# Optimization experiments

Measured on AMD Instinct MI355X. Metric: run time of the kernel, lower is better.

The kernel has to match this reference:

```python
import jax, jax.numpy as jnp
import numpy as np

N = 4_194_304      # number of coordinate samples
H = 4              # hidden_features
L = 256            # hidden_layers
FIRST_OMEGA = 3000.0
HIDDEN_OMEGA = 30.0


def setup_inputs() -> dict:
    key = jax.random.key(0)
    ks = jax.random.split(key, 11)
    coords = jax.random.normal(ks[0], (N, 1), dtype=jnp.float32)
    # first layer: weight uniform(-1/in_features, 1/in_features), in_features=1
    w_first = jax.random.uniform(ks[1], (H, 1), jnp.float32, -1.0, 1.0)
    b_first = jax.random.uniform(ks[2], (H,), jnp.float32, -1.0, 1.0)
    # hidden layers: uniform(-sqrt(6/H)/omega, +)
    c_hid = float(np.sqrt(6.0 / H) / HIDDEN_OMEGA)
    w_hidden = jax.random.uniform(ks[3], (L, H, H), jnp.float32, -c_hid, c_hid)
    b_hidden = jax.random.uniform(ks[4], (L, H), jnp.float32, -c_hid, c_hid)
    # outermost linear, same init const
    w_out = jax.random.uniform(ks[5], (1, H), jnp.float32, -c_hid, c_hid)
    b_out = jax.random.uniform(ks[6], (1,), jnp.float32, -c_hid, c_hid)
    # harmonizer scalars (a,b,c,d); near 0 so exp(a)~1
    a_param = (jax.random.normal(ks[7], (), jnp.float32) * 0.1)
    b_param = (jax.random.normal(ks[8], (), jnp.float32) * 0.1)
    c_param = (jax.random.normal(ks[9], (), jnp.float32) * 0.1)
    d_param = (jax.random.normal(ks[10], (), jnp.float32) * 0.1)
    return {
        "coords": coords,
        "w_first": w_first, "b_first": b_first,
        "w_hidden": w_hidden, "b_hidden": b_hidden,
        "w_out": w_out, "b_out": b_out,
        "a_param": a_param, "b_param": b_param,
        "c_param": c_param, "d_param": d_param,
    }


def reference(coords, w_first, b_first, w_hidden, b_hidden, w_out, b_out,
              a_param, b_param, c_param, d_param):
    amp = jnp.exp(a_param)
    freq = jnp.exp(b_param)
    # first sine layer, omega_0 = 3000
    x = amp * jnp.sin(freq * FIRST_OMEGA * (coords @ w_first.T + b_first) + c_param) + d_param
    # 256 hidden sine layers, omega_0 = 30, via scan over the stacked weights
    def step(h, wb):
        W, bvec = wb  # W: [H,H], bvec: [H]
        h = amp * jnp.sin(freq * HIDDEN_OMEGA * (h @ W.T + bvec) + c_param) + d_param
        return h, None
    x, _ = jax.lax.scan(step, x, (w_hidden, b_hidden))
    # outermost plain linear
    return x @ w_out.T + b_out
```

## Files before the change

### kernel.cpp

```cpp
#include <hip/hip_runtime.h>
#include <math.h>

#define NSAMP 4194304
#define LAYERS 256
#define SPT 8


__global__ void prep_kernel(
    const float* __restrict__ w_hidden, const float* __restrict__ b_hidden,
    const float* __restrict__ w_out,   const float* __restrict__ b_out,
    const float* __restrict__ a_param, const float* __restrict__ b_param,
    const float* __restrict__ c_param, const float* __restrict__ d_param,
    float* __restrict__ ws)
{
  const double TWO_PI = 6.283185307179586476925286766559;
  int idx = blockIdx.x * blockDim.x + threadIdx.x;
  float freqf = (float)exp((double)b_param[0]);
  float gf = (float)((double)freqf * 30.0);
  double scale = (double)gf / TWO_PI;
  if (idx < 4096) {
    ws[16 + idx] = (float)((double)w_hidden[idx] * scale);
  } else if (idx < 5120) {
    int bi = idx - 4096;
    ws[16 + 4096 + bi] =
        (float)(((double)gf * (double)b_hidden[bi] + (double)c_param[0]) / TWO_PI);
  } else if (idx == 5120) {
    ws[0] = (float)exp((double)a_param[0]);
    ws[1] = d_param[0];
    ws[2] = (float)((double)freqf * 3000.0);
    ws[3] = c_param[0];
    ws[4] = b_out[0];
    ws[5] = w_out[0]; ws[6] = w_out[1]; ws[7] = w_out[2]; ws[8] = w_out[3];
  }
}

#if defined(__has_builtin)
#if __has_builtin(__builtin_amdgcn_sinf)
#define HAVE_SINF_BUILTIN 1
#endif
#endif

__device__ __forceinline__ float vsin_rev(float x) {
#ifdef HAVE_SINF_BUILTIN
  return __builtin_amdgcn_sinf(x);
#else
  float r;
  asm("v_sin_f32 %0, %1" : "=v"(r) : "v"(x));
  return r;
#endif
}

__device__ __forceinline__ float sin_first(float A) {
  double x = (double)A;
  double kd = rint(x * 0.31830988618379067154);
  double r  = fma(-kd, 3.1415926535897931159979634685, x);
  r = fma(-kd, 1.2246467991473531772e-16, r);
  double r2 = r * r;
  double p = 1.6059043836821613e-10;
  p = fma(r2, p, -2.5052108385441718775e-8);
  p = fma(r2, p,  2.7557319223985890653e-6);
  p = fma(r2, p, -1.9841269841269841270e-4);
  p = fma(r2, p,  8.3333333333333333333e-3);
  p = fma(r2, p, -1.6666666666666666667e-1);
  double s = fma(r2 * r, p, r);
  int ki = (int)kd;
  if (ki & 1) s = -s;
  return (float)s;
}

__global__ __launch_bounds__(256) void siren_main(
    const float* __restrict__ coords,
    const float* __restrict__ w_first, const float* __restrict__ b_first,
    const float* __restrict__ ws, float* __restrict__ out)
{
  const int tid = blockIdx.x * blockDim.x + threadIdx.x;
  const float amp = ws[0], dpar = ws[1], f3000 = ws[2], cpar = ws[3];

  float c[SPT];
  const float4* cp4 = reinterpret_cast<const float4*>(coords) + tid * (SPT / 4);
#pragma unroll
  for (int q = 0; q < SPT / 4; ++q) {
    float4 v = cp4[q];
    c[4*q+0] = v.x; c[4*q+1] = v.y; c[4*q+2] = v.z; c[4*q+3] = v.w;
  }

  float h[SPT][4];
#pragma unroll
  for (int s = 0; s < SPT; ++s) {
#pragma unroll
    for (int i = 0; i < 4; ++i) {
      float t = __fmul_rn(c[s], w_first[i]);
      t = __fadd_rn(t, b_first[i]);
      float A = __fadd_rn(__fmul_rn(f3000, t), cpar);
      float sn = sin_first(A);
      h[s][i] = __fadd_rn(__fmul_rn(amp, sn), dpar);
    }
  }

  const float* __restrict__ Wp = ws + 16;
  const float* __restrict__ Bp = ws + 16 + 4096;

  for (int l = 0; l < LAYERS; ++l) {
    float w[16], b4[4];
#pragma unroll
    for (int k = 0; k < 16; ++k) w[k] = Wp[l * 16 + k];
#pragma unroll
    for (int k = 0; k < 4; ++k) b4[k] = Bp[l * 4 + k];
#pragma unroll
    for (int s = 0; s < SPT; ++s) {
      float z[4];
#pragma unroll
      for (int i = 0; i < 4; ++i) {
        float acc = b4[i];
#pragma unroll
        for (int j = 0; j < 4; ++j) acc = fmaf(w[i * 4 + j], h[s][j], acc);
        z[i] = acc;
      }
#pragma unroll
      for (int i = 0; i < 4; ++i) {
        float sn = vsin_rev(z[i]);
        h[s][i] = __fadd_rn(__fmul_rn(amp, sn), dpar);
      }
    }
  }

  const float wo0 = ws[5], wo1 = ws[6], wo2 = ws[7], wo3 = ws[8], bo = ws[4];
  float o[SPT];
#pragma unroll
  for (int s = 0; s < SPT; ++s) {
    float acc = fmaf(h[s][0], wo0, bo);
    acc = fmaf(h[s][1], wo1, acc);
    acc = fmaf(h[s][2], wo2, acc);
    acc = fmaf(h[s][3], wo3, acc);
    o[s] = acc;
  }
  float4* op4 = reinterpret_cast<float4*>(out) + tid * (SPT / 4);
#pragma unroll
  for (int q = 0; q < SPT / 4; ++q) {
    float4 v;
    v.x = o[4*q+0]; v.y = o[4*q+1]; v.z = o[4*q+2]; v.w = o[4*q+3];
    op4[q] = v;
  }
}

extern "C" void kernel_launch(void* const* d_in, const int* in_sizes, int n_in,
                              void* d_out, int out_size, void* d_ws, size_t ws_size,
                              hipStream_t stream) {
  const float* coords   = (const float*)d_in[0];
  const float* w_first  = (const float*)d_in[1];
  const float* b_first  = (const float*)d_in[2];
  const float* w_hidden = (const float*)d_in[3];
  const float* b_hidden = (const float*)d_in[4];
  const float* w_out    = (const float*)d_in[5];
  const float* b_out    = (const float*)d_in[6];
  const float* a_param  = (const float*)d_in[7];
  const float* b_param  = (const float*)d_in[8];
  const float* c_param  = (const float*)d_in[9];
  const float* d_param  = (const float*)d_in[10];
  float* ws   = (float*)d_ws;
  float* outp = (float*)d_out;

  prep_kernel<<<21, 256, 0, stream>>>(w_hidden, b_hidden, w_out, b_out,
                                      a_param, b_param, c_param, d_param, ws);

  const int threads = NSAMP / SPT;
  siren_main<<<threads / 256, 256, 0, stream>>>(coords, w_first, b_first, ws, outp);
}
```

Measured before the change: 785.9 us.

## Fold amp/d into weights and use packed-FP32 polynomial sine for hidden layers

```diff
diff --git a/kernel.cpp b/kernel.cpp
--- a/kernel.cpp
+++ b/kernel.cpp
@@ -5,6 +5,15 @@
 #define LAYERS 256
 #define SPT 8
 
+typedef float f32x2 __attribute__((ext_vector_type(2)));
+
+__device__ __forceinline__ f32x2 splat2(float v) { f32x2 r = {v, v}; return r; }
+__device__ __forceinline__ f32x2 vfma2(f32x2 a, f32x2 b, f32x2 c) {
+  return __builtin_elementwise_fma(a, b, c);
+}
+
+#define WS_W2 16
+#define WS_B2 8208
 
 __global__ void prep_kernel(
     const float* __restrict__ w_hidden, const float* __restrict__ b_hidden,
@@ -16,38 +25,36 @@
   const double TWO_PI = 6.283185307179586476925286766559;
   int idx = blockIdx.x * blockDim.x + threadIdx.x;
   float freqf = (float)exp((double)b_param[0]);
-  float gf = (float)((double)freqf * 30.0);
+  float gf    = (float)((double)freqf * 30.0);
+  float ampf  = (float)exp((double)a_param[0]);
   double scale = (double)gf / TWO_PI;
+  double dd = (double)d_param[0];
   if (idx < 4096) {
-    ws[16 + idx] = (float)((double)w_hidden[idx] * scale);
+    float wv = (float)((double)w_hidden[idx] * scale * (double)ampf);
+    ws[WS_W2 + 2*idx]     = wv;
+    ws[WS_W2 + 2*idx + 1] = wv;
   } else if (idx < 5120) {
     int bi = idx - 4096;
-    ws[16 + 4096 + bi] =
-        (float)(((double)gf * (double)b_hidden[bi] + (double)c_param[0]) / TWO_PI);
+    int l = bi >> 2, i = bi & 3;
+    double rs = 0.0;
+    for (int j = 0; j < 4; ++j) rs += (double)w_hidden[l*16 + i*4 + j];
+    double bv = ((double)gf * (double)b_hidden[bi] + (double)c_param[0]) / TWO_PI
+              + dd * scale * rs;
+    float b = (float)bv;
+    ws[WS_B2 + 2*bi]     = b;
+    ws[WS_B2 + 2*bi + 1] = b;
   } else if (idx == 5120) {
-    ws[0] = (float)exp((double)a_param[0]);
-    ws[1] = d_param[0];
-    ws[2] = (float)((double)freqf * 3000.0);
-    ws[3] = c_param[0];
-    ws[4] = b_out[0];
-    ws[5] = w_out[0]; ws[6] = w_out[1]; ws[7] = w_out[2]; ws[8] = w_out[3];
+    ws[0] = (float)((double)freqf * 3000.0);
+    ws[1] = c_param[0];
+    double bo = (double)b_out[0]
+              + dd * ((double)w_out[0] + (double)w_out[1] +
+                      (double)w_out[2] + (double)w_out[3]);
+    ws[2] = (float)bo;
+    ws[3] = (float)((double)ampf * (double)w_out[0]);
+    ws[4] = (float)((double)ampf * (double)w_out[1]);
+    ws[5] = (float)((double)ampf * (double)w_out[2]);
+    ws[6] = (float)((double)ampf * (double)w_out[3]);
   }
-}
-
-#if defined(__has_builtin)
-#if __has_builtin(__builtin_amdgcn_sinf)
-#define HAVE_SINF_BUILTIN 1
-#endif
-#endif
-
-__device__ __forceinline__ float vsin_rev(float x) {
-#ifdef HAVE_SINF_BUILTIN
-  return __builtin_amdgcn_sinf(x);
-#else
-  float r;
-  asm("v_sin_f32 %0, %1" : "=v"(r) : "v"(x));
-  return r;
-#endif
 }
 
 __device__ __forceinline__ float sin_first(float A) {
@@ -68,13 +75,30 @@
   return (float)s;
 }
 
+__device__ __forceinline__ f32x2 sin_rev2(f32x2 z) {
+  f32x2 n;
+  n.x = rintf(z.x);
+  n.y = rintf(z.y);
+  f32x2 r  = z - n;
+  f32x2 r2 = r * r;
+  f32x2 p  = splat2(-0.7181225f);
+  p = vfma2(p, r2, splat2( 3.8199536f));
+  p = vfma2(p, r2, splat2(-15.0946469f));
+  p = vfma2(p, r2, splat2( 42.058693944897630f));
+  p = vfma2(p, r2, splat2(-76.705859753061358f));
+  p = vfma2(p, r2, splat2( 81.605249276075034f));
+  p = vfma2(p, r2, splat2(-41.341702240399755f));
+  p = vfma2(p, r2, splat2( 6.2831853071795865f));
+  return r * p;
+}
+
 __global__ __launch_bounds__(256) void siren_main(
     const float* __restrict__ coords,
     const float* __restrict__ w_first, const float* __restrict__ b_first,
     const float* __restrict__ ws, float* __restrict__ out)
 {
   const int tid = blockIdx.x * blockDim.x + threadIdx.x;
-  const float amp = ws[0], dpar = ws[1], f3000 = ws[2], cpar = ws[3];
+  const float f3000 = ws[0], cpar = ws[1];
 
   float c[SPT];
   const float4* cp4 = reinterpret_cast<const float4*>(coords) + tid * (SPT / 4);
@@ -84,63 +108,62 @@
     c[4*q+0] = v.x; c[4*q+1] = v.y; c[4*q+2] = v.z; c[4*q+3] = v.w;
   }
 
-  float h[SPT][4];
+  float wf[4], bf[4];
+#pragma unroll
+  for (int i = 0; i < 4; ++i) { wf[i] = w_first[i]; bf[i] = b_first[i]; }
+
+  f32x2 sp[SPT/2][4];
 #pragma unroll
   for (int s = 0; s < SPT; ++s) {
 #pragma unroll
     for (int i = 0; i < 4; ++i) {
-      float t = __fmul_rn(c[s], w_first[i]);
-      t = __fadd_rn(t, b_first[i]);
+      float t = __fmul_rn(c[s], wf[i]);
+      t = __fadd_rn(t, bf[i]);
       float A = __fadd_rn(__fmul_rn(f3000, t), cpar);
-      float sn = sin_first(A);
-      h[s][i] = __fadd_rn(__fmul_rn(amp, sn), dpar);
+      sp[s >> 1][i][s & 1] = sin_first(A);
     }
   }
 
-  const float* __restrict__ Wp = ws + 16;
-  const float* __restrict__ Bp = ws + 16 + 4096;
+  const f32x2* __restrict__ W2 = reinterpret_cast<const f32x2*>(ws + WS_W2);
+  const f32x2* __restrict__ B2 = reinterpret_cast<const f32x2*>(ws + WS_B2);
 
   for (int l = 0; l < LAYERS; ++l) {
-    float w[16], b4[4];
+    f32x2 wv[16], bv[4];
 #pragma unroll
-    for (int k = 0; k < 16; ++k) w[k] = Wp[l * 16 + k];
+    for (int k = 0; k < 16; ++k) wv[k] = W2[l * 16 + k];
 #pragma unroll
-    for (int k = 0; k < 4; ++k) b4[k] = Bp[l * 4 + k];
+    for (int i = 0; i < 4; ++i) bv[i] = B2[l * 4 + i];
 #pragma unroll
-    for (int s = 0; s < SPT; ++s) {
-      float z[4];
+    for (int p = 0; p < SPT/2; ++p) {
+      f32x2 z[4];
 #pragma unroll
       for (int i = 0; i < 4; ++i) {
-        float acc = b4[i];
+        z[i] = vfma2(wv[i*4+0], sp[p][0], bv[i]);
 #pragma unroll
-        for (int j = 0; j < 4; ++j) acc = fmaf(w[i * 4 + j], h[s][j], acc);
-        z[i] = acc;
+        for (int j = 1; j < 4; ++j) z[i] = vfma2(wv[i*4+j], sp[p][j], z[i]);
       }
 #pragma unroll
-      for (int i = 0; i < 4; ++i) {
-        float sn = vsin_rev(z[i]);
-        h[s][i] = __fadd_rn(__fmul_rn(amp, sn), dpar);
-      }
+      for (int i = 0; i < 4; ++i) sp[p][i] = sin_rev2(z[i]);
     }
   }
 
-  const float wo0 = ws[5], wo1 = ws[6], wo2 = ws[7], wo3 = ws[8], bo = ws[4];
-  float o[SPT];
+  const f32x2 wo0 = splat2(ws[3]), wo1 = splat2(ws[4]);
+  const f32x2 wo2 = splat2(ws[5]), wo3 = splat2(ws[6]);
+  const f32x2 bo  = splat2(ws[2]);
+  f32x2 o[SPT/2];
 #pragma unroll
-  for (int s = 0; s < SPT; ++s) {
-    float acc = fmaf(h[s][0], wo0, bo);
-    acc = fmaf(h[s][1], wo1, acc);
-    acc = fmaf(h[s][2], wo2, acc);
-    acc = fmaf(h[s][3], wo3, acc);
-    o[s] = acc;
+  for (int p = 0; p < SPT/2; ++p) {
+    f32x2 acc = vfma2(wo0, sp[p][0], bo);
+    acc = vfma2(wo1, sp[p][1], acc);
+    acc = vfma2(wo2, sp[p][2], acc);
+    acc = vfma2(wo3, sp[p][3], acc);
+    o[p] = acc;
   }
   float4* op4 = reinterpret_cast<float4*>(out) + tid * (SPT / 4);
-#pragma unroll
-  for (int q = 0; q < SPT / 4; ++q) {
-    float4 v;
-    v.x = o[4*q+0]; v.y = o[4*q+1]; v.z = o[4*q+2]; v.w = o[4*q+3];
-    op4[q] = v;
-  }
+  float4 v0 = { o[0].x, o[0].y, o[1].x, o[1].y };
+  float4 v1 = { o[2].x, o[2].y, o[3].x, o[3].y };
+  op4[0] = v0;
+  op4[1] = v1;
 }
 
 extern "C" void kernel_launch(void* const* d_in, const int* in_sizes, int n_in,
```

Measured after the change: 986.5 us. 1.26x slower.

## Fold amp and d into hidden weights/biases and double-buffer per-layer weight loads

Applied to the files above, without the earlier changes.

```diff
diff --git a/kernel.cpp b/kernel.cpp
--- a/kernel.cpp
+++ b/kernel.cpp
@@ -5,6 +5,7 @@
 #define LAYERS 256
 #define SPT 8
 
+#define WS_W 16
 
 __global__ void prep_kernel(
     const float* __restrict__ w_hidden, const float* __restrict__ b_hidden,
@@ -16,21 +17,33 @@
   const double TWO_PI = 6.283185307179586476925286766559;
   int idx = blockIdx.x * blockDim.x + threadIdx.x;
   float freqf = (float)exp((double)b_param[0]);
-  float gf = (float)((double)freqf * 30.0);
+  float gf    = (float)((double)freqf * 30.0);
+  float ampf  = (float)exp((double)a_param[0]);
   double scale = (double)gf / TWO_PI;
+  double dd = (double)d_param[0];
   if (idx < 4096) {
-    ws[16 + idx] = (float)((double)w_hidden[idx] * scale);
+    int l = idx >> 4, r = idx & 15;
+    float wv = (float)((double)w_hidden[idx] * scale * (double)ampf);
+    ws[WS_W + l * 20 + r] = wv;
   } else if (idx < 5120) {
     int bi = idx - 4096;
-    ws[16 + 4096 + bi] =
-        (float)(((double)gf * (double)b_hidden[bi] + (double)c_param[0]) / TWO_PI);
+    int l = bi >> 2, i = bi & 3;
+    double rs = 0.0;
+    for (int j = 0; j < 4; ++j) rs += (double)w_hidden[l*16 + i*4 + j];
+    double bv = ((double)gf * (double)b_hidden[bi] + (double)c_param[0]) / TWO_PI
+              + dd * scale * rs;
+    ws[WS_W + l * 20 + 16 + i] = (float)bv;
   } else if (idx == 5120) {
-    ws[0] = (float)exp((double)a_param[0]);
-    ws[1] = d_param[0];
-    ws[2] = (float)((double)freqf * 3000.0);
-    ws[3] = c_param[0];
-    ws[4] = b_out[0];
-    ws[5] = w_out[0]; ws[6] = w_out[1]; ws[7] = w_out[2]; ws[8] = w_out[3];
+    ws[0] = (float)((double)freqf * 3000.0);
+    ws[1] = c_param[0];
+    double bo = (double)b_out[0]
+              + dd * ((double)w_out[0] + (double)w_out[1] +
+                      (double)w_out[2] + (double)w_out[3]);
+    ws[2] = (float)bo;
+    ws[3] = (float)((double)ampf * (double)w_out[0]);
+    ws[4] = (float)((double)ampf * (double)w_out[1]);
+    ws[5] = (float)((double)ampf * (double)w_out[2]);
+    ws[6] = (float)((double)ampf * (double)w_out[3]);
   }
 }
 
@@ -74,7 +87,7 @@
     const float* __restrict__ ws, float* __restrict__ out)
 {
   const int tid = blockIdx.x * blockDim.x + threadIdx.x;
-  const float amp = ws[0], dpar = ws[1], f3000 = ws[2], cpar = ws[3];
+  const float f3000 = ws[0], cpar = ws[1];
 
   float c[SPT];
   const float4* cp4 = reinterpret_cast<const float4*>(coords) + tid * (SPT / 4);
@@ -84,63 +97,84 @@
     c[4*q+0] = v.x; c[4*q+1] = v.y; c[4*q+2] = v.z; c[4*q+3] = v.w;
   }
 
-  float h[SPT][4];
+  float wf[4], bf[4];
+#pragma unroll
+  for (int i = 0; i < 4; ++i) { wf[i] = w_first[i]; bf[i] = b_first[i]; }
+
+  float sp[SPT][4];
 #pragma unroll
   for (int s = 0; s < SPT; ++s) {
 #pragma unroll
     for (int i = 0; i < 4; ++i) {
-      float t = __fmul_rn(c[s], w_first[i]);
-      t = __fadd_rn(t, b_first[i]);
+      float t = __fmul_rn(c[s], wf[i]);
+      t = __fadd_rn(t, bf[i]);
       float A = __fadd_rn(__fmul_rn(f3000, t), cpar);
-      float sn = sin_first(A);
-      h[s][i] = __fadd_rn(__fmul_rn(amp, sn), dpar);
+      sp[s][i] = sin_first(A);
     }
   }
 
-  const float* __restrict__ Wp = ws + 16;
-  const float* __restrict__ Bp = ws + 16 + 4096;
-
-  for (int l = 0; l < LAYERS; ++l) {
-    float w[16], b4[4];
-#pragma unroll
-    for (int k = 0; k < 16; ++k) w[k] = Wp[l * 16 + k];
-#pragma unroll
-    for (int k = 0; k < 4; ++k) b4[k] = Bp[l * 4 + k];
-#pragma unroll
-    for (int s = 0; s < SPT; ++s) {
-      float z[4];
-#pragma unroll
-      for (int i = 0; i < 4; ++i) {
-        float acc = b4[i];
-#pragma unroll
-        for (int j = 0; j < 4; ++j) acc = fmaf(w[i * 4 + j], h[s][j], acc);
-        z[i] = acc;
-      }
-#pragma unroll
-      for (int i = 0; i < 4; ++i) {
-        float sn = vsin_rev(z[i]);
-        h[s][i] = __fadd_rn(__fmul_rn(amp, sn), dpar);
-      }
+  const float* __restrict__ Wb = ws + WS_W;
+
+#define STEP(WREG)                                                      \
+  {                                                                     \
+    _Pragma("unroll")                                                   \
+    for (int s = 0; s < SPT; ++s) {                                     \
+      float z0 = fmaf(WREG[0],  sp[s][0], WREG[16]);                    \
+      z0 = fmaf(WREG[1],  sp[s][1], z0);                                \
+      z0 = fmaf(WREG[2],  sp[s][2], z0);                                \
+      z0 = fmaf(WREG[3],  sp[s][3], z0);                                \
+      float z1 = fmaf(WREG[4],  sp[s][0], WREG[17]);                    \
+      z1 = fmaf(WREG[5],  sp[s][1], z1);                                \
+      z1 = fmaf(WREG[6],  sp[s][2], z1);                                \
+      z1 = fmaf(WREG[7],  sp[s][3], z1);                                \
+      float z2 = fmaf(WREG[8],  sp[s][0], WREG[18]);                    \
+      z2 = fmaf(WREG[9],  sp[s][1], z2);                                \
+      z2 = fmaf(WREG[10], sp[s][2], z2);                                \
+      z2 = fmaf(WREG[11], sp[s][3], z2);                                \
+      float z3 = fmaf(WREG[12], sp[s][0], WREG[19]);                    \
+      z3 = fmaf(WREG[13], sp[s][1], z3);                                \
+      z3 = fmaf(WREG[14], sp[s][2], z3);                                \
+      z3 = fmaf(WREG[15], sp[s][3], z3);                                \
+      sp[s][0] = vsin_rev(z0);                                          \
+      sp[s][1] = vsin_rev(z1);                                          \
+      sp[s][2] = vsin_rev(z2);                                          \
+      sp[s][3] = vsin_rev(z3);                                          \
+    }                                                                   \
+  }
+
+  float wA[20], wB[20];
+#pragma unroll
+  for (int k = 0; k < 20; ++k) wA[k] = Wb[k];
+
+  for (int l = 0; l < LAYERS; l += 2) {
+    const float* p1 = Wb + (l + 1) * 20;
+#pragma unroll
+    for (int k = 0; k < 20; ++k) wB[k] = p1[k];
+    STEP(wA);
+    if (l + 2 < LAYERS) {
+      const float* p2 = Wb + (l + 2) * 20;
+#pragma unroll
+      for (int k = 0; k < 20; ++k) wA[k] = p2[k];
     }
-  }
-
-  const float wo0 = ws[5], wo1 = ws[6], wo2 = ws[7], wo3 = ws[8], bo = ws[4];
+    STEP(wB);
+  }
+#undef STEP
+
+  const float wo0 = ws[3], wo1 = ws[4], wo2 = ws[5], wo3 = ws[6], bo = ws[2];
   float o[SPT];
 #pragma unroll
   for (int s = 0; s < SPT; ++s) {
-    float acc = fmaf(h[s][0], wo0, bo);
-    acc = fmaf(h[s][1], wo1, acc);
-    acc = fmaf(h[s][2], wo2, acc);
-    acc = fmaf(h[s][3], wo3, acc);
+    float acc = fmaf(sp[s][0], wo0, bo);
+    acc = fmaf(sp[s][1], wo1, acc);
+    acc = fmaf(sp[s][2], wo2, acc);
+    acc = fmaf(sp[s][3], wo3, acc);
     o[s] = acc;
   }
   float4* op4 = reinterpret_cast<float4*>(out) + tid * (SPT / 4);
-#pragma unroll
-  for (int q = 0; q < SPT / 4; ++q) {
-    float4 v;
-    v.x = o[4*q+0]; v.y = o[4*q+1]; v.z = o[4*q+2]; v.w = o[4*q+3];
-    op4[q] = v;
-  }
+  float4 v0 = { o[0], o[1], o[2], o[3] };
+  float4 v1 = { o[4], o[5], o[6], o[7] };
+  op4[0] = v0;
+  op4[1] = v1;
 }
 
 extern "C" void kernel_launch(void* const* d_in, const int* in_sizes, int n_in,
```

After: 723.8 us, median of 2. -7.9%, faster.
